# Kernel tuning notes

Measured on AMD Instinct MI355X. Metric: run time of the kernel, lower is better.

The kernel has to match this reference:

```python
import jax, jax.numpy as jnp
import numpy as np

# 3D multi-scale deformable attention (MSDeformAttn, n_heads=8 / 3D variant)
LEVEL_SHAPES = [(32, 32, 32), (16, 16, 16), (8, 8, 8), (4, 4, 4)]  # (H, W, D) per level
D_MODEL, N_HEADS, N_LEVELS, N_POINTS = 256, 8, 4, 4
C_HEAD = D_MODEL // N_HEADS  # 32
N_BATCH, LEN_Q = 1, 37440
LEN_IN = sum(h * w * d for h, w, d in LEVEL_SHAPES)  # 37440


def setup_inputs() -> dict:
    key = jax.random.key(0)
    ks = jax.random.split(key, 10)
    s = 0.02  # param init scale
    return {
        "query": jax.random.normal(ks[0], (N_BATCH, LEN_Q, D_MODEL), jnp.float32),
        "reference_points": jax.random.uniform(ks[1], (N_BATCH, LEN_Q, N_LEVELS, 3), jnp.float32),
        "input_flatten": jax.random.normal(ks[2], (N_BATCH, LEN_IN, D_MODEL), jnp.float32),
        "input_spatial_shapes": jnp.array(LEVEL_SHAPES, dtype=jnp.int32),
        "input_level_start_index": jnp.array(
            np.cumsum([0] + [h * w * d for h, w, d in LEVEL_SHAPES])[:-1], dtype=jnp.int32),
        "W_value": s * jax.random.normal(ks[3], (D_MODEL, D_MODEL), jnp.float32),
        "b_value": jnp.zeros((D_MODEL,), jnp.float32),
        "W_off": s * jax.random.normal(ks[4], (D_MODEL, N_HEADS * N_LEVELS * N_POINTS * 3), jnp.float32),
        "b_off": s * jax.random.normal(ks[5], (N_HEADS * N_LEVELS * N_POINTS * 3,), jnp.float32),
        "W_attn": s * jax.random.normal(ks[6], (D_MODEL, N_HEADS * N_LEVELS * N_POINTS), jnp.float32),
        "b_attn": jnp.zeros((N_HEADS * N_LEVELS * N_POINTS,), jnp.float32),
        "W_out": s * jax.random.normal(ks[7], (D_MODEL, D_MODEL), jnp.float32),
        "b_out": jnp.zeros((D_MODEL,), jnp.float32),
    }


def trilinear_sample(vol, gx, gy, gz):
    """torch F.grid_sample 3D, mode=bilinear, padding=zeros, align_corners=False.
    vol: (B, C, Dz, Dy, Dx); gx indexes Dx, gy indexes Dy, gz indexes Dz, each (B, Q) in [-1,1].
    Returns (B, C, Q)."""
    B, C, Dz, Dy, Dx = vol.shape
    ix = ((gx + 1.0) * Dx - 1.0) * 0.5
    iy = ((gy + 1.0) * Dy - 1.0) * 0.5
    iz = ((gz + 1.0) * Dz - 1.0) * 0.5
    x0f, y0f, z0f = jnp.floor(ix), jnp.floor(iy), jnp.floor(iz)
    fx, fy, fz = ix - x0f, iy - y0f, iz - z0f
    x0, y0, z0 = x0f.astype(jnp.int32), y0f.astype(jnp.int32), z0f.astype(jnp.int32)
    vol_f = vol.reshape(B, C, Dz * Dy * Dx)
    out = jnp.zeros((B, C, gx.shape[1]), vol.dtype)
    for dz in (0, 1):
        for dy in (0, 1):
            for dx in (0, 1):
                xc, yc, zc = x0 + dx, y0 + dy, z0 + dz
                w = ((fx if dx else 1.0 - fx) * (fy if dy else 1.0 - fy) * (fz if dz else 1.0 - fz))
                valid = ((xc >= 0) & (xc < Dx) & (yc >= 0) & (yc < Dy) & (zc >= 0) & (zc < Dz))
                idx = (jnp.clip(zc, 0, Dz - 1) * Dy + jnp.clip(yc, 0, Dy - 1)) * Dx + jnp.clip(xc, 0, Dx - 1)
                v = jnp.take_along_axis(vol_f, idx[:, None, :], axis=2)  # (B, C, Q)
                out = out + (w * valid.astype(w.dtype))[:, None, :] * v
    return out


def reference(query, reference_points, input_flatten, input_spatial_shapes,
              input_level_start_index, W_value, b_value, W_off, b_off,
              W_attn, b_attn, W_out, b_out):
    N, Lq, _ = query.shape
    Lin = input_flatten.shape[1]
    value = (input_flatten @ W_value + b_value).reshape(N, Lin, N_HEADS, C_HEAD)
    off = (query @ W_off + b_off).reshape(N, Lq, N_HEADS, N_LEVELS, N_POINTS, 3)
    attn = jax.nn.softmax((query @ W_attn + b_attn).reshape(N, Lq, N_HEADS, N_LEVELS * N_POINTS), axis=-1)
    # offset_normalizer = [W, H, D] per level (as in the torch code)
    norm = jnp.stack([input_spatial_shapes[:, 1], input_spatial_shapes[:, 0],
                      input_spatial_shapes[:, 2]], -1).astype(query.dtype)
    loc = reference_points[:, :, None, :, None, :] + off / norm[None, None, None, :, None, :]
    grids = 2.0 * loc - 1.0  # (N, Lq, M, L, P, 3)
    starts = np.cumsum([0] + [h * w * d for h, w, d in LEVEL_SHAPES])
    sampled = []
    for l, (H, W, D) in enumerate(LEVEL_SHAPES):
        vl = value[:, starts[l]:starts[l + 1]]  # (N, H*W*D, M, C)
        vol = (vl.reshape(N, H, W, D, N_HEADS, C_HEAD)
                 .transpose(0, 4, 5, 1, 2, 3)
                 .reshape(N * N_HEADS, C_HEAD, H, W, D))
        g = grids[:, :, :, l].transpose(0, 2, 1, 3, 4).reshape(N * N_HEADS, Lq * N_POINTS, 3)
        # grid x indexes last vol dim (D), y indexes W, z indexes H (torch grid_sample convention)
        s = trilinear_sample(vol, g[..., 0], g[..., 1], g[..., 2])  # (N*M, C, Lq*P)
        sampled.append(s.reshape(N * N_HEADS, C_HEAD, Lq, N_POINTS))
    samp = jnp.stack(sampled, axis=-2).reshape(N * N_HEADS, C_HEAD, Lq, N_LEVELS * N_POINTS)
    aw = attn.transpose(0, 2, 1, 3).reshape(N * N_HEADS, 1, Lq, N_LEVELS * N_POINTS)
    out = (samp * aw).sum(-1).reshape(N, N_HEADS * C_HEAD, Lq).transpose(0, 2, 1)
    return out @ W_out + b_out
```

## Files before the change

kernel.cpp:

```cpp
#include <hip/hip_runtime.h>
#include <math.h>

#define LQ      37440
#define LIN     37440
#define DMODEL  256
#define NHEADS  8
#define CHEAD   32
#define K_DIM   256

typedef __attribute__((ext_vector_type(8))) short short8;
typedef __attribute__((ext_vector_type(4))) short short4v;
typedef __attribute__((ext_vector_type(4))) float f32x4;
typedef __attribute__((ext_vector_type(2))) float f32x2;

__device__ inline unsigned short bf16_rte(float f) {
    union { float f; unsigned u; } v; v.f = f;
    return (unsigned short)((v.u + 0x7fffu + ((v.u >> 16) & 1u)) >> 16);
}
__device__ inline float bf16_f(unsigned short s) {
    union { unsigned u; float f; } v; v.u = ((unsigned)s) << 16;
    return v.f;
}
__device__ inline float bits_f(unsigned u) {
    union { unsigned u; float f; } v; v.u = u;
    return v.f;
}
__device__ inline unsigned pkbf(float a, float b) {
    return (unsigned)bf16_rte(a) | ((unsigned)bf16_rte(b) << 16);
}

__device__ __forceinline__ void gl_lds16(const unsigned short* g, unsigned short* l) {
    __builtin_amdgcn_global_load_lds(
        (const __attribute__((address_space(1))) void*)g,
        (__attribute__((address_space(3))) void*)l, 16, 0, 0);
}

__global__ __launch_bounds__(256) void prep_all(
        const float* __restrict__ inp, const float* __restrict__ query,
        const float* __restrict__ Wv, const float* __restrict__ Wo,
        const float* __restrict__ Wa, const float* __restrict__ Wout,
        const float* __restrict__ bo, const float* __restrict__ ba,
        unsigned short* __restrict__ in_b, unsigned short* __restrict__ q_b,
        unsigned short* __restrict__ Bv, unsigned short* __restrict__ Bq,
        unsigned short* __restrict__ Bw, float* __restrict__ bias_m, int n4)
{
    const int bid = blockIdx.x;
    if (bid < 18720) {
        int i = bid * 256 + threadIdx.x;
        const float* src;
        unsigned short* dst;
        int j;
        if (i < n4) { src = inp;   dst = in_b; j = i; }
        else        { src = query; dst = q_b;  j = i - n4; }
        float4 v = ((const float4*)src)[j];
        short4v h;
        h.x = (short)bf16_rte(v.x);
        h.y = (short)bf16_rte(v.y);
        h.z = (short)bf16_rte(v.z);
        h.w = (short)bf16_rte(v.w);
        ((short4v*)dst)[j] = h;
    } else {
        int i = (bid - 18720) * 256 + threadIdx.x;
        int n = i >> 8, k = i & 255;
        if (n < 256) {
            Bv[(size_t)n * 256 + k] = bf16_rte(Wv[(size_t)k * 256 + n]);
        } else if (n < 640) {
            int m = n - 256;
            Bq[(size_t)m * 256 + k] = bf16_rte(Wo[(size_t)k * 384 + m]);
        } else if (n < 768) {
            int m = n - 640;
            Bq[(size_t)(384 + m) * 256 + k] = bf16_rte(Wa[(size_t)k * 128 + m]);
        } else {
            int m = n - 768;
            Bw[(size_t)m * 256 + k] = bf16_rte(Wout[(size_t)k * 256 + m]);
        }
        if (i < 512) bias_m[i] = (i < 384) ? bo[i] : ba[i - 384];
    }
}

__global__ __launch_bounds__(256) void gemm2(
    const unsigned short* __restrict__ in_b, const unsigned short* __restrict__ q_b,
    const unsigned short* __restrict__ Bv,   const unsigned short* __restrict__ Bq,
    const float* __restrict__ bv, const float* __restrict__ bias_m,
    unsigned short* __restrict__ value_t, unsigned short* __restrict__ qbuf)
{
    __shared__ __align__(16) unsigned short AsL[128 * 32];
    __shared__ __align__(16) unsigned short BsL[128 * 32];

    const int t    = threadIdx.x;
    const int bm   = blockIdx.y * 128;
    const int w    = t >> 6;
    const int lane = t & 63;
    const int lm   = lane & 15;
    const int quad = lane >> 4;

    const int isval = (blockIdx.x < 2);
    const unsigned short* A  = isval ? in_b : q_b;
    const unsigned short* Bt = isval ? Bv : Bq;
    const float* bias        = isval ? bv : bias_m;
    const int n0             = (isval ? blockIdx.x : (blockIdx.x - 2)) * 128;

    const unsigned short* ga[2]; unsigned short* la[2];
    const unsigned short* gb[2]; unsigned short* lb[2];
    #pragma unroll
    for (int i = 0; i < 2; ++i) {
        int idx = i * 256 + t;
        int row = idx >> 2;
        int chn = (idx & 3) ^ ((row >> 1) & 3);
        int rga = bm + row; if (rga >= LQ) rga = LQ - 1;
        ga[i] = A  + (size_t)rga * K_DIM + chn * 8;
        gb[i] = Bt + (size_t)(n0 + row) * K_DIM + chn * 8;
        la[i] = AsL + i * 2048 + (t >> 6) * 512;
        lb[i] = BsL + i * 2048 + (t >> 6) * 512;
    }

    const int ra0 = w * 32 + lm, ra1 = ra0 + 16;
    const int aoff0 = ra0 * 32 + ((quad ^ ((ra0 >> 1) & 3)) << 3);
    const int aoff1 = ra1 * 32 + ((quad ^ ((ra1 >> 1) & 3)) << 3);
    int boff[8];
    #pragma unroll
    for (int nt = 0; nt < 8; ++nt) {
        int rb = nt * 16 + lm;
        boff[nt] = rb * 32 + ((quad ^ ((rb >> 1) & 3)) << 3);
    }

    f32x4 acc[2][8];
    #pragma unroll
    for (int mt = 0; mt < 2; ++mt)
        #pragma unroll
        for (int nt = 0; nt < 8; ++nt)
            acc[mt][nt] = (f32x4){0.f, 0.f, 0.f, 0.f};

    for (int k0 = 0; k0 < K_DIM; k0 += 32) {
        __syncthreads();
        gl_lds16(ga[0] + k0, la[0]);
        gl_lds16(ga[1] + k0, la[1]);
        gl_lds16(gb[0] + k0, lb[0]);
        gl_lds16(gb[1] + k0, lb[1]);
        __syncthreads();

        short8 af[2], bf[8];
        af[0] = *(const short8*)&AsL[aoff0];
        af[1] = *(const short8*)&AsL[aoff1];
        #pragma unroll
        for (int nt = 0; nt < 8; ++nt)
            bf[nt] = *(const short8*)&BsL[boff[nt]];
        #pragma unroll
        for (int mt = 0; mt < 2; ++mt)
            #pragma unroll
            for (int nt = 0; nt < 8; ++nt)
                acc[mt][nt] = __builtin_amdgcn_mfma_f32_16x16x32_bf16(af[mt], bf[nt], acc[mt][nt], 0, 0, 0);
    }

    #pragma unroll
    for (int nt = 0; nt < 8; ++nt) {
        int col = n0 + nt * 16 + lm;
        float bb = bias[col];
        #pragma unroll
        for (int mt = 0; mt < 2; ++mt)
            #pragma unroll
            for (int r = 0; r < 4; ++r) {
                int row = bm + w * 32 + mt * 16 + quad * 4 + r;
                if (row < LQ) {
                    float o = acc[mt][nt][r] + bb;
                    if (isval) {
                        int h = col >> 5, c = col & 31;
                        value_t[((size_t)h * LIN + row) * 32 + c] = bf16_rte(o);
                    } else {
                        qbuf[(size_t)row * 512 + col] = bf16_rte(o);
                    }
                }
            }
    }
}

__global__ __launch_bounds__(256) void gemm_out(
    const unsigned short* __restrict__ A, const unsigned short* __restrict__ Bt,
    const float* __restrict__ bias, float* __restrict__ Cout)
{
    __shared__ __align__(16) unsigned short AsL[128 * 32];
    __shared__ __align__(16) unsigned short BsL[128 * 32];

    const int t    = threadIdx.x;
    const int bm   = blockIdx.y * 128;
    const int n0   = blockIdx.x * 128;
    const int w    = t >> 6;
    const int lane = t & 63;
    const int lm   = lane & 15;
    const int quad = lane >> 4;

    const unsigned short* ga[2]; unsigned short* la[2];
    const unsigned short* gb[2]; unsigned short* lb[2];
    #pragma unroll
    for (int i = 0; i < 2; ++i) {
        int idx = i * 256 + t;
        int row = idx >> 2;
        int chn = (idx & 3) ^ ((row >> 1) & 3);
        int rga = bm + row; if (rga >= LQ) rga = LQ - 1;
        ga[i] = A  + (size_t)rga * K_DIM + chn * 8;
        gb[i] = Bt + (size_t)(n0 + row) * K_DIM + chn * 8;
        la[i] = AsL + i * 2048 + (t >> 6) * 512;
        lb[i] = BsL + i * 2048 + (t >> 6) * 512;
    }

    const int ra0 = w * 32 + lm, ra1 = ra0 + 16;
    const int aoff0 = ra0 * 32 + ((quad ^ ((ra0 >> 1) & 3)) << 3);
    const int aoff1 = ra1 * 32 + ((quad ^ ((ra1 >> 1) & 3)) << 3);
    int boff[8];
    #pragma unroll
    for (int nt = 0; nt < 8; ++nt) {
        int rb = nt * 16 + lm;
        boff[nt] = rb * 32 + ((quad ^ ((rb >> 1) & 3)) << 3);
    }

    f32x4 acc[2][8];
    #pragma unroll
    for (int mt = 0; mt < 2; ++mt)
        #pragma unroll
        for (int nt = 0; nt < 8; ++nt)
            acc[mt][nt] = (f32x4){0.f, 0.f, 0.f, 0.f};

    for (int k0 = 0; k0 < K_DIM; k0 += 32) {
        __syncthreads();
        gl_lds16(ga[0] + k0, la[0]);
        gl_lds16(ga[1] + k0, la[1]);
        gl_lds16(gb[0] + k0, lb[0]);
        gl_lds16(gb[1] + k0, lb[1]);
        __syncthreads();

        short8 af[2], bf[8];
        af[0] = *(const short8*)&AsL[aoff0];
        af[1] = *(const short8*)&AsL[aoff1];
        #pragma unroll
        for (int nt = 0; nt < 8; ++nt)
            bf[nt] = *(const short8*)&BsL[boff[nt]];
        #pragma unroll
        for (int mt = 0; mt < 2; ++mt)
            #pragma unroll
            for (int nt = 0; nt < 8; ++nt)
                acc[mt][nt] = __builtin_amdgcn_mfma_f32_16x16x32_bf16(af[mt], bf[nt], acc[mt][nt], 0, 0, 0);
    }

    #pragma unroll
    for (int nt = 0; nt < 8; ++nt) {
        int col = n0 + nt * 16 + lm;
        float bb = bias[col];
        #pragma unroll
        for (int mt = 0; mt < 2; ++mt)
            #pragma unroll
            for (int r = 0; r < 4; ++r) {
                int row = bm + w * 32 + mt * 16 + quad * 4 + r;
                if (row < LQ)
                    Cout[(size_t)row * DMODEL + col] = acc[mt][nt][r] + bb;
            }
    }
}

__global__ __launch_bounds__(256) void sample_kernel(
    const float* __restrict__ refp,
    const unsigned short* __restrict__ qbuf,
    const unsigned short* __restrict__ value_t,
    unsigned short* __restrict__ samp)
{
    __shared__ float4 zywS[4][16][8];
    __shared__ f32x2  wxS [4][16][8];
    __shared__ int4   ozyS[4][16][8];

    const int t  = threadIdx.x;
    const int q0 = blockIdx.x * 4;

    const int   Sz[4]   = {32, 16, 8, 4};
    const float invS[4] = {1.f/32.f, 1.f/16.f, 1.f/8.f, 1.f/4.f};
    const int   St[4]   = {0, 32768, 36864, 37376};

    #pragma unroll
    for (int pi = t; pi < 512; pi += 256) {
        int ql = pi >> 7;
        int hp = pi & 127;
        int hh = hp >> 4;
        int c  = hp & 15;
        int l  = c >> 2;
        int q  = q0 + ql;
        const unsigned short* o = qbuf + (size_t)q * 512 + hp * 3;
        const float* r = refp + q * 12 + l * 3;
        const int   S  = Sz[l];
        const float Sf = (float)S;
        const float is = invS[l];
        float ix = (r[0] + bf16_f(o[0]) * is) * Sf - 0.5f;
        float iy = (r[1] + bf16_f(o[1]) * is) * Sf - 0.5f;
        float iz = (r[2] + bf16_f(o[2]) * is) * Sf - 0.5f;
        float xf = floorf(ix), yf = floorf(iy), zf = floorf(iz);
        float fx = ix - xf, fy = iy - yf, fz = iz - zf;
        int x0 = (int)xf, y0 = (int)yf, z0 = (int)zf;

        float wx0 = (x0 >= 0  && x0 < S)     ? (1.f - fx) : 0.f;
        float wx1 = (x0 >= -1 && x0 < S - 1) ? fx         : 0.f;
        float wy0 = (y0 >= 0  && y0 < S)     ? (1.f - fy) : 0.f;
        float wy1 = (y0 >= -1 && y0 < S - 1) ? fy         : 0.f;
        float wz0 = (z0 >= 0  && z0 < S)     ? (1.f - fz) : 0.f;
        float wz1 = (z0 >= -1 && z0 < S - 1) ? fz         : 0.f;

        int cy0 = min(max(y0, 0), S - 1), cy1 = min(max(y0 + 1, 0), S - 1);
        int cz0 = min(max(z0, 0), S - 1), cz1 = min(max(z0 + 1, 0), S - 1);

        float lgv = bf16_f(qbuf[(size_t)q * 512 + 384 + hp]);
        float m = fmaxf(lgv, __shfl_xor(lgv, 1));
        m = fmaxf(m, __shfl_xor(m, 2));
        m = fmaxf(m, __shfl_xor(m, 4));
        m = fmaxf(m, __shfl_xor(m, 8));
        float e = __expf(lgv - m);
        float s = e + __shfl_xor(e, 1);
        s += __shfl_xor(s, 2);
        s += __shfl_xor(s, 4);
        s += __shfl_xor(s, 8);
        float a = __fdividef(e, s);

        const int S2 = S * S;
        const int st = St[l];
        const int xb = x0 * 32;
        zywS[ql][c][hh] = make_float4(wz0*wy0, wz0*wy1, wz1*wy0, wz1*wy1);
        wxS [ql][c][hh] = (f32x2){wx0 * a, wx1 * a};
        ozyS[ql][c][hh] = make_int4((st + cz0*S2 + cy0*S) * 32 + xb,
                                    (st + cz0*S2 + cy1*S) * 32 + xb,
                                    (st + cz1*S2 + cy0*S) * 32 + xb,
                                    (st + cz1*S2 + cy1*S) * 32 + xb);
    }
    __syncthreads();

    const int ql   = t >> 6;
    const int lane = t & 63;
    const int hh   = lane >> 3;
    const int j    = lane & 7;
    const int xsel = j >> 2;
    const int cgrp = (j & 3) << 3;
    const int q    = q0 + ql;

    const unsigned short* vbase = value_t - 64;
    const unsigned laneoff = (unsigned)(hh * (LIN * 32) + j * 8 + 64);

    f32x2 acc0 = {0.f,0.f}, acc1 = {0.f,0.f}, acc2 = {0.f,0.f}, acc3 = {0.f,0.f};

    #pragma unroll
    for (int c = 0; c < 16; ++c) {
        float4 zyw = zywS[ql][c][hh];
        f32x2  wx  = wxS [ql][c][hh];
        int4   zo  = ozyS[ql][c][hh];
        float  ws  = xsel ? wx.y : wx.x;

        #define CORNER(OFF, WZ) { \
            int4 v = *(const int4*)(vbase + (laneoff + (unsigned)(OFF))); \
            float w_ = (WZ) * ws; \
            f32x2 w2 = {w_, w_}; \
            acc0 += w2 * (f32x2){bits_f(((unsigned)v.x) << 16), bits_f((unsigned)v.x)}; \
            acc1 += w2 * (f32x2){bits_f(((unsigned)v.y) << 16), bits_f((unsigned)v.y)}; \
            acc2 += w2 * (f32x2){bits_f(((unsigned)v.z) << 16), bits_f((unsigned)v.z)}; \
            acc3 += w2 * (f32x2){bits_f(((unsigned)v.w) << 16), bits_f((unsigned)v.w)}; }

        CORNER(zo.x, zyw.x);
        CORNER(zo.y, zyw.y);
        CORNER(zo.z, zyw.z);
        CORNER(zo.w, zyw.w);
        #undef CORNER
    }

    float c0 = acc0.x + __shfl_xor(acc0.x, 4);
    float c1 = acc0.y + __shfl_xor(acc0.y, 4);
    float c2 = acc1.x + __shfl_xor(acc1.x, 4);
    float c3 = acc1.y + __shfl_xor(acc1.y, 4);
    float c4 = acc2.x + __shfl_xor(acc2.x, 4);
    float c5 = acc2.y + __shfl_xor(acc2.y, 4);
    float c6 = acc3.x + __shfl_xor(acc3.x, 4);
    float c7 = acc3.y + __shfl_xor(acc3.y, 4);
    if (xsel == 0) {
        int4 o = make_int4((int)pkbf(c0, c1), (int)pkbf(c2, c3),
                           (int)pkbf(c4, c5), (int)pkbf(c6, c7));
        *(int4*)(samp + (size_t)q * DMODEL + hh * CHEAD + cgrp) = o;
    }
}

extern "C" void kernel_launch(void* const* d_in, const int* in_sizes, int n_in,
                              void* d_out, int out_size, void* d_ws, size_t ws_size,
                              hipStream_t stream) {
    const float* query = (const float*)d_in[0];
    const float* refp  = (const float*)d_in[1];
    const float* inp   = (const float*)d_in[2];
    const float* Wv   = (const float*)d_in[5];
    const float* bv   = (const float*)d_in[6];
    const float* Wo   = (const float*)d_in[7];
    const float* bo   = (const float*)d_in[8];
    const float* Wa   = (const float*)d_in[9];
    const float* ba   = (const float*)d_in[10];
    const float* Wout = (const float*)d_in[11];
    const float* bout = (const float*)d_in[12];

    char* p = (char*)d_ws;
    p += 256;
    unsigned short* value_t = (unsigned short*)p; p += (size_t)LIN * 256 * 2;
    unsigned short* qbuf    = (unsigned short*)p; p += (size_t)LQ * 512 * 2;
    unsigned short* samp    = (unsigned short*)p; p += (size_t)LQ * 256 * 2;
    unsigned short* in_b    = (unsigned short*)p; p += (size_t)LQ * 256 * 2;
    unsigned short* q_b     = (unsigned short*)p; p += (size_t)LQ * 256 * 2;
    unsigned short* Bv   = (unsigned short*)p;    p += 256 * 256 * 2;
    unsigned short* Bq   = (unsigned short*)p;    p += 512 * 256 * 2;
    unsigned short* Bw   = (unsigned short*)p;    p += 256 * 256 * 2;
    float* bias_m = (float*)p;                    p += 512 * 4;

    const int n4 = LQ * 256 / 4;
    dim3 blk(256);

    prep_all<<<18720 + 1024, blk, 0, stream>>>(
        inp, query, Wv, Wo, Wa, Wout, bo, ba,
        in_b, q_b, Bv, Bq, Bw, bias_m, n4);
    gemm2<<<dim3(6, (LQ + 127) / 128), blk, 0, stream>>>(
        in_b, q_b, Bv, Bq, bv, bias_m, value_t, qbuf);
    sample_kernel<<<LQ / 4, blk, 0, stream>>>(refp, qbuf, value_t, samp);
    gemm_out<<<dim3(2, (LQ + 127) / 128), blk, 0, stream>>>(samp, Bw, bout, (float*)d_out);
}
```

Baseline: 348.8 us.

## Double-buffer GEMM LDS staging and add shifted value copy for aligned sampling

Both GEMM kernels now use two LDS buffers, prefetching the next K-slice with global_load_lds while computing the current one. This replaces the two full barriers per iteration with vmcnt waits. Separately, the value GEMM writes a second copy of value_t shifted by 32 elements, and the sampler picks that copy for odd x0. The x0/x0+1 corner pair then presumably starts at an aligned boundary so it can be loaded as a wider chunk. The cost is an extra full value write (about 19 MB) and more workspace, plus padding zeroed in prep.

Result: faster. 322.7 us (-7.5%).

```diff
diff --git a/kernel.cpp b/kernel.cpp
--- a/kernel.cpp
+++ b/kernel.cpp
@@ -7,6 +7,8 @@
 #define NHEADS  8
 #define CHEAD   32
 #define K_DIM   256
+
+#define VALB_DELTA (LIN * 256 + 32)
 
 typedef __attribute__((ext_vector_type(8))) short short8;
 typedef __attribute__((ext_vector_type(4))) short short4v;
@@ -42,7 +44,10 @@
         const float* __restrict__ bo, const float* __restrict__ ba,
         unsigned short* __restrict__ in_b, unsigned short* __restrict__ q_b,
         unsigned short* __restrict__ Bv, unsigned short* __restrict__ Bq,
-        unsigned short* __restrict__ Bw, float* __restrict__ bias_m, int n4)
+        unsigned short* __restrict__ Bw, float* __restrict__ bias_m,
+        unsigned short* __restrict__ padA,
+        unsigned short* __restrict__ valB,
+        int n4)
 {
     const int bid = blockIdx.x;
     if (bid < 18720) {
@@ -75,6 +80,9 @@
             Bw[(size_t)m * 256 + k] = bf16_rte(Wout[(size_t)k * 256 + m]);
         }
         if (i < 512) bias_m[i] = (i < 384) ? bo[i] : ba[i - 384];
+        if (i < 64)       padA[i] = 0;
+        else if (i < 96)  valB[i - 64] = 0;
+        else if (i < 192) valB[(size_t)LIN * 256 + 32 + (i - 96)] = 0;
     }
 }
 
@@ -82,10 +90,11 @@
     const unsigned short* __restrict__ in_b, const unsigned short* __restrict__ q_b,
     const unsigned short* __restrict__ Bv,   const unsigned short* __restrict__ Bq,
     const float* __restrict__ bv, const float* __restrict__ bias_m,
-    unsigned short* __restrict__ value_t, unsigned short* __restrict__ qbuf)
+    unsigned short* __restrict__ value_t, unsigned short* __restrict__ valB,
+    unsigned short* __restrict__ qbuf)
 {
-    __shared__ __align__(16) unsigned short AsL[128 * 32];
-    __shared__ __align__(16) unsigned short BsL[128 * 32];
+    __shared__ __align__(16) unsigned short AsL[2 * 4096];
+    __shared__ __align__(16) unsigned short BsL[2 * 4096];
 
     const int t    = threadIdx.x;
     const int bm   = blockIdx.y * 128;
@@ -100,8 +109,8 @@
     const float* bias        = isval ? bv : bias_m;
     const int n0             = (isval ? blockIdx.x : (blockIdx.x - 2)) * 128;
 
-    const unsigned short* ga[2]; unsigned short* la[2];
-    const unsigned short* gb[2]; unsigned short* lb[2];
+    const unsigned short* ga[2]; const unsigned short* gb[2];
+    int loff[2];
     #pragma unroll
     for (int i = 0; i < 2; ++i) {
         int idx = i * 256 + t;
@@ -110,8 +119,7 @@
         int rga = bm + row; if (rga >= LQ) rga = LQ - 1;
         ga[i] = A  + (size_t)rga * K_DIM + chn * 8;
         gb[i] = Bt + (size_t)(n0 + row) * K_DIM + chn * 8;
-        la[i] = AsL + i * 2048 + (t >> 6) * 512;
-        lb[i] = BsL + i * 2048 + (t >> 6) * 512;
+        loff[i] = i * 2048 + w * 512;
     }
 
     const int ra0 = w * 32 + lm, ra1 = ra0 + 16;
@@ -131,26 +139,42 @@
         for (int nt = 0; nt < 8; ++nt)
             acc[mt][nt] = (f32x4){0.f, 0.f, 0.f, 0.f};
 
-    for (int k0 = 0; k0 < K_DIM; k0 += 32) {
-        __syncthreads();
-        gl_lds16(ga[0] + k0, la[0]);
-        gl_lds16(ga[1] + k0, la[1]);
-        gl_lds16(gb[0] + k0, lb[0]);
-        gl_lds16(gb[1] + k0, lb[1]);
-        __syncthreads();
-
+    #define STAGE(K0, SEL) do { \
+        gl_lds16(ga[0] + (K0), AsL + (SEL) * 4096 + loff[0]); \
+        gl_lds16(ga[1] + (K0), AsL + (SEL) * 4096 + loff[1]); \
+        gl_lds16(gb[0] + (K0), BsL + (SEL) * 4096 + loff[0]); \
+        gl_lds16(gb[1] + (K0), BsL + (SEL) * 4096 + loff[1]); \
+    } while (0)
+
+    STAGE(0, 0);
+    #pragma unroll
+    for (int kt = 0; kt < 8; ++kt) {
+        const int sel = kt & 1;
+        if (kt < 7) {
+            STAGE((kt + 1) * 32, sel ^ 1);
+            asm volatile("s_waitcnt vmcnt(4)" ::: "memory");
+        } else {
+            asm volatile("s_waitcnt vmcnt(0)" ::: "memory");
+        }
+        __builtin_amdgcn_s_barrier();
+
+        const int so = sel * 4096;
         short8 af[2], bf[8];
-        af[0] = *(const short8*)&AsL[aoff0];
-        af[1] = *(const short8*)&AsL[aoff1];
+        af[0] = *(const short8*)&AsL[so + aoff0];
+        af[1] = *(const short8*)&AsL[so + aoff1];
         #pragma unroll
         for (int nt = 0; nt < 8; ++nt)
-            bf[nt] = *(const short8*)&BsL[boff[nt]];
+            bf[nt] = *(const short8*)&BsL[so + boff[nt]];
         #pragma unroll
         for (int mt = 0; mt < 2; ++mt)
             #pragma unroll
             for (int nt = 0; nt < 8; ++nt)
                 acc[mt][nt] = __builtin_amdgcn_mfma_f32_16x16x32_bf16(af[mt], bf[nt], acc[mt][nt], 0, 0, 0);
-    }
+
+        asm volatile("s_waitcnt lgkmcnt(0)" ::: "memory");
+        __builtin_amdgcn_s_barrier();
+    }
+    #undef STAGE
 
     #pragma unroll
     for (int nt = 0; nt < 8; ++nt) {
@@ -165,7 +189,10 @@
                     float o = acc[mt][nt][r] + bb;
                     if (isval) {
                         int h = col >> 5, c = col & 31;
-                        value_t[((size_t)h * LIN + row) * 32 + c] = bf16_rte(o);
+                        unsigned short vb = bf16_rte(o);
+                        size_t e = ((size_t)h * LIN + row) * 32 + c;
+                        value_t[e] = vb;
+                        valB[32 + e] = vb;
                     } else {
                         qbuf[(size_t)row * 512 + col] = bf16_rte(o);
                     }
@@ -178,8 +205,8 @@
     const unsigned short* __restrict__ A, const unsigned short* __restrict__ Bt,
     const float* __restrict__ bias, float* __restrict__ Cout)
 {
-    __shared__ __align__(16) unsigned short AsL[128 * 32];
-    __shared__ __align__(16) unsigned short BsL[128 * 32];
+    __shared__ __align__(16) unsigned short AsL[2 * 4096];
+    __shared__ __align__(16) unsigned short BsL[2 * 4096];
 
     const int t    = threadIdx.x;
     const int bm   = blockIdx.y * 128;
@@ -189,8 +216,8 @@
     const int lm   = lane & 15;
     const int quad = lane >> 4;
 
-    const unsigned short* ga[2]; unsigned short* la[2];
-    const unsigned short* gb[2]; unsigned short* lb[2];
+    const unsigned short* ga[2]; const unsigned short* gb[2];
+    int loff[2];
     #pragma unroll
     for (int i = 0; i < 2; ++i) {
         int idx = i * 256 + t;
@@ -199,8 +226,7 @@
         int rga = bm + row; if (rga >= LQ) rga = LQ - 1;
         ga[i] = A  + (size_t)rga * K_DIM + chn * 8;
         gb[i] = Bt + (size_t)(n0 + row) * K_DIM + chn * 8;
-        la[i] = AsL + i * 2048 + (t >> 6) * 512;
-        lb[i] = BsL + i * 2048 + (t >> 6) * 512;
+        loff[i] = i * 2048 + w * 512;
     }
 
     const int ra0 = w * 32 + lm, ra1 = ra0 + 16;
@@ -220,26 +246,42 @@
         for (int nt = 0; nt < 8; ++nt)
             acc[mt][nt] = (f32x4){0.f, 0.f, 0.f, 0.f};
 
-    for (int k0 = 0; k0 < K_DIM; k0 += 32) {
-        __syncthreads();
-        gl_lds16(ga[0] + k0, la[0]);
-        gl_lds16(ga[1] + k0, la[1]);
-        gl_lds16(gb[0] + k0, lb[0]);
-        gl_lds16(gb[1] + k0, lb[1]);
-        __syncthreads();
-
+    #define STAGE(K0, SEL) do { \
+        gl_lds16(ga[0] + (K0), AsL + (SEL) * 4096 + loff[0]); \
+        gl_lds16(ga[1] + (K0), AsL + (SEL) * 4096 + loff[1]); \
+        gl_lds16(gb[0] + (K0), BsL + (SEL) * 4096 + loff[0]); \
+        gl_lds16(gb[1] + (K0), BsL + (SEL) * 4096 + loff[1]); \
+    } while (0)
+
+    STAGE(0, 0);
+    #pragma unroll
+    for (int kt = 0; kt < 8; ++kt) {
+        const int sel = kt & 1;
+        if (kt < 7) {
+            STAGE((kt + 1) * 32, sel ^ 1);
+            asm volatile("s_waitcnt vmcnt(4)" ::: "memory");
+        } else {
+            asm volatile("s_waitcnt vmcnt(0)" ::: "memory");
+        }
+        __builtin_amdgcn_s_barrier();
+
+        const int so = sel * 4096;
         short8 af[2], bf[8];
-        af[0] = *(const short8*)&AsL[aoff0];
-        af[1] = *(const short8*)&AsL[aoff1];
+        af[0] = *(const short8*)&AsL[so + aoff0];
+        af[1] = *(const short8*)&AsL[so + aoff1];
         #pragma unroll
         for (int nt = 0; nt < 8; ++nt)
-            bf[nt] = *(const short8*)&BsL[boff[nt]];
+            bf[nt] = *(const short8*)&BsL[so + boff[nt]];
         #pragma unroll
         for (int mt = 0; mt < 2; ++mt)
             #pragma unroll
             for (int nt = 0; nt < 8; ++nt)
                 acc[mt][nt] = __builtin_amdgcn_mfma_f32_16x16x32_bf16(af[mt], bf[nt], acc[mt][nt], 0, 0, 0);
-    }
+
+        asm volatile("s_waitcnt lgkmcnt(0)" ::: "memory");
+        __builtin_amdgcn_s_barrier();
+    }
+    #undef STAGE
 
     #pragma unroll
     for (int nt = 0; nt < 8; ++nt) {
@@ -317,7 +359,7 @@
 
         const int S2 = S * S;
         const int st = St[l];
-        const int xb = x0 * 32;
+        const int xb = x0 * 32 + ((x0 & 1) ? VALB_DELTA : 0);
         zywS[ql][c][hh] = make_float4(wz0*wy0, wz0*wy1, wz1*wy0, wz1*wy1);
         wxS [ql][c][hh] = (f32x2){wx0 * a, wx1 * a};
         ozyS[ql][c][hh] = make_int4((st + cz0*S2 + cy0*S) * 32 + xb,
@@ -396,6 +438,7 @@
     char* p = (char*)d_ws;
     p += 256;
     unsigned short* value_t = (unsigned short*)p; p += (size_t)LIN * 256 * 2;
+    unsigned short* valB    = (unsigned short*)p; p += ((size_t)LIN * 256 + 128) * 2;
     unsigned short* qbuf    = (unsigned short*)p; p += (size_t)LQ * 512 * 2;
     unsigned short* samp    = (unsigned short*)p; p += (size_t)LQ * 256 * 2;
     unsigned short* in_b    = (unsigned short*)p; p += (size_t)LQ * 256 * 2;
@@ -410,9 +453,9 @@
 
     prep_all<<<18720 + 1024, blk, 0, stream>>>(
         inp, query, Wv, Wo, Wa, Wout, bo, ba,
-        in_b, q_b, Bv, Bq, Bw, bias_m, n4);
+        in_b, q_b, Bv, Bq, Bw, bias_m, value_t - 64, valB, n4);
     gemm2<<<dim3(6, (LQ + 127) / 128), blk, 0, stream>>>(
-        in_b, q_b, Bv, Bq, bv, bias_m, value_t, qbuf);
+        in_b, q_b, Bv, Bq, bv, bias_m, value_t, valB, qbuf);
     sample_kernel<<<LQ / 4, blk, 0, stream>>>(refp, qbuf, value_t, samp);
     gemm_out<<<dim3(2, (LQ + 127) / 128), blk, 0, stream>>>(samp, Bw, bout, (float*)d_out);
 }
```
